# Optimization experiments

Measured on AMD Instinct MI355X. Metric: run time of the kernel, lower is better.

Reference implementation:

```python
import jax, jax.numpy as jnp
import numpy as np

CUTOFF = 3.5          # angular_cutoff (init kwarg)
EPS = 1e-7            # keras.backend.epsilon()
CLIP_MIN = 1e-10      # tf.clip_by_value min on Carnot denominators
B, N = 8, 32
MLP_DIMS = [(9, 64), (64, 64), (64, 64), (64, 64), (64, 64), (64, 128), (128, 256)]


def _he(key, fan_in, fan_out):
    return jax.random.normal(key, (fan_in, fan_out), jnp.float32) * np.float32(np.sqrt(2.0 / fan_in))


def setup_inputs() -> dict:
    key = jax.random.key(0)
    k_pos, k_sp, k_w, k_b = jax.random.split(key, 4)
    # realistic symmetric distance matrix with zero diagonal, from random 3D positions
    pos = jax.random.uniform(k_pos, (B, N, 3), jnp.float32) * 9.0
    diff = pos[:, :, None, :] - pos[:, None, :, :]
    D = jnp.sqrt(jnp.sum(diff * diff, axis=-1) + 1e-12)
    D = D * (1.0 - jnp.eye(N, dtype=jnp.float32))
    species = jax.random.randint(k_sp, (B, N), 1, 10).astype(jnp.float32)
    inp = {"distance_matrices": D, "num_species_batch": species}
    for i, (fi, fo) in enumerate(MLP_DIMS):
        inp[f"W{i}"] = _he(jax.random.fold_in(k_w, i), fi, fo)
        inp[f"b{i}"] = jax.random.normal(jax.random.fold_in(k_b, i), (fo,), jnp.float32) * 0.01
    return inp


def _ang_mlp(x, W0, b0, W1, b1, W2, b2, W3, b3, W4, b4, W5, b5, W6, b6):
    # residual MLP: 9 -> 64 (x5, two residual adds) -> 128 -> 256, all tanh
    x_res = jnp.tanh(x @ W0 + b0)
    x1 = jnp.tanh(x_res @ W1 + b1)
    xb1 = x1 + x_res
    x2 = jnp.tanh(xb1 @ W2 + b2)
    x3 = jnp.tanh(x2 @ W3 + b3)
    x4 = jnp.tanh(x3 @ W4 + b4)
    xb2 = x4 + xb1
    xb3 = jnp.tanh(xb2 @ W5 + b5)
    return jnp.tanh(xb3 @ W6 + b6)


def _forward(D, S, W0, b0, W1, b1, W2, b2, W3, b3, W4, b4, W5, b5, W6, b6):
    n = D.shape[-1]
    ji, ki = jnp.triu_indices(n, k=1)                       # P = n(n-1)/2 ordered pairs j<k
    cm = (D < CUTOFF) & (D != 0.0)                          # [B,N,N]
    mask = cm[:, :, ji] & cm[:, :, ki]                      # [B,N,P] valid triplets (i;j,k)
    R_ij = D[:, :, ji]                                      # [B,N,P]
    R_ik = D[:, :, ki]
    R_jk = jnp.broadcast_to(D[:, ji, ki][:, None, :], R_ij.shape)
    z_i = jnp.broadcast_to(S[:, :, None], R_ij.shape)
    z_j = jnp.broadcast_to(S[:, ji][:, None, :], R_ij.shape)
    z_k = jnp.broadcast_to(S[:, ki][:, None, :], R_ij.shape)
    # Carnot formula for the three cosines of the triangle (i,j,k)
    clip = lambda d: jnp.maximum(d, CLIP_MIN)
    c_i = (R_ij**2 + R_ik**2 - R_jk**2) / clip(2.0 * R_ij * R_ik)
    c_j = (R_ij**2 + R_jk**2 - R_ik**2) / clip(2.0 * R_ij * R_jk)
    c_k = (R_ik**2 + R_jk**2 - R_ij**2) / clip(2.0 * R_ik * R_jk)
    geo = jnp.stack([
        R_ij + R_ik + R_jk,
        R_ij * R_ik + R_ij * R_jk + R_ik * R_jk,
        R_ij * R_ik * R_jk,
    ], axis=-1)                                             # [B,N,P,3]
    chem = jnp.stack([
        z_i + z_j + z_k,
        c_i + c_j + c_k,
        z_i * (z_j + z_k) + z_j * z_k - c_i * (c_j + c_k) - c_j * c_k,
        z_i * (c_j + c_k) + c_i * (z_j + z_k) + z_j * c_k + c_j * z_k,
        z_i * (z_j * z_k - c_j * c_k) - c_i * (z_j * c_k + c_j * z_k),
        z_i * (z_j * c_k + c_j * z_k) + c_i * (z_j * z_k - c_j * c_k),
    ], axis=-1)                                             # [B,N,P,6]
    geo = geo / (jnp.linalg.norm(geo, axis=-1, keepdims=True) + EPS)
    chem = chem / (jnp.linalg.norm(chem, axis=-1, keepdims=True) + EPS)
    feat = jnp.concatenate([geo, chem], axis=-1)            # [B,N,P,9]
    out = _ang_mlp(feat, W0, b0, W1, b1, W2, b2, W3, b3, W4, b4, W5, b5, W6, b6)  # [B,N,P,256]
    f_c = lambda d: 0.5 * jnp.cos(np.float32(np.pi) * d / CUTOFF) + 0.5
    w = jnp.where(mask, f_c(R_ij) * f_c(R_ik), 0.0)[..., None]
    GA = jnp.sum(out * w, axis=2)                           # scatter-add over triplets -> [B,N,256]
    return GA / (jnp.linalg.norm(GA, axis=-1, keepdims=True) + EPS)


def reference(distance_matrices, num_species_batch, W0, b0, W1, b1, W2, b2, W3, b3, W4, b4, W5, b5, W6, b6):
    return _forward(distance_matrices, num_species_batch, W0, b0, W1, b1, W2, b2, W3, b3, W4, b4, W5, b5, W6, b6)
```

## Files before the change

### kernel.cpp

```cpp
#include <hip/hip_runtime.h>
#include <math.h>

#define NB 8
#define NA 32
#define NCELL 256
#define NPAIR 496
#define SLOT 496
#define FST 10
#define TC 16
#define XS 20
#define NQ 8
#define CUTOFF_F 3.5f
#define EPS_F 1e-7f
#define CLIP_MIN_F 1e-10f
#define PI_F 3.14159274101257324f

__global__ __launch_bounds__(256) void aev_feat(
    const float* __restrict__ D, const float* __restrict__ S,
    float* __restrict__ feat, int* __restrict__ count, float* __restrict__ GA)
{
    __shared__ float Dm[NA][NA];
    __shared__ float Sv[NA];
    __shared__ int s_T;
    const int tid = threadIdx.x;
    const int cell = blockIdx.x;
    const int b = cell >> 5, i = cell & 31;

    for (int idx = tid; idx < NA * NA; idx += 256)
        ((float*)Dm)[idx] = D[b * NA * NA + idx];
    if (tid < NA) Sv[tid] = S[b * NA + tid];
    if (tid == 0) s_T = 0;
    GA[cell * 256 + tid] = 0.f;
    __syncthreads();

    for (int p = tid; p < NPAIR; p += 256) {
        int rem = p, j = 0;
        while (rem >= 31 - j) { rem -= 31 - j; ++j; }
        const int k = j + 1 + rem;
        const float dij = Dm[i][j], dik = Dm[i][k];
        if (dij < CUTOFF_F && dij != 0.f && dik < CUTOFF_F && dik != 0.f) {
            const int slot = atomicAdd(&s_T, 1);
            const float Rij = dij, Rik = dik, Rjk = Dm[j][k];
            const float zi = Sv[i], zj = Sv[j], zk = Sv[k];
            const float ci = (Rij*Rij + Rik*Rik - Rjk*Rjk) / fmaxf(2.f*Rij*Rik, CLIP_MIN_F);
            const float cj = (Rij*Rij + Rjk*Rjk - Rik*Rik) / fmaxf(2.f*Rij*Rjk, CLIP_MIN_F);
            const float ck = (Rik*Rik + Rjk*Rjk - Rij*Rij) / fmaxf(2.f*Rik*Rjk, CLIP_MIN_F);
            float g0 = Rij + Rik + Rjk;
            float g1 = Rij*Rik + Rij*Rjk + Rik*Rjk;
            float g2 = Rij*Rik*Rjk;
            const float gn = sqrtf(g0*g0 + g1*g1 + g2*g2) + EPS_F;
            float h0 = zi + zj + zk;
            float h1 = ci + cj + ck;
            float h2 = zi*(zj + zk) + zj*zk - ci*(cj + ck) - cj*ck;
            float h3 = zi*(cj + ck) + ci*(zj + zk) + zj*ck + cj*zk;
            float h4 = zi*(zj*zk - cj*ck) - ci*(zj*ck + cj*zk);
            float h5 = zi*(zj*ck + cj*zk) + ci*(zj*zk - cj*ck);
            const float hn = sqrtf(h0*h0 + h1*h1 + h2*h2 + h3*h3 + h4*h4 + h5*h5) + EPS_F;
            const float fcij = 0.5f * cosf(PI_F * Rij / CUTOFF_F) + 0.5f;
            const float fcik = 0.5f * cosf(PI_F * Rik / CUTOFF_F) + 0.5f;
            float* fp = &feat[(cell * SLOT + slot) * FST];
            fp[0] = g0 / gn; fp[1] = g1 / gn; fp[2] = g2 / gn;
            fp[3] = h0 / hn; fp[4] = h1 / hn; fp[5] = h2 / hn;
            fp[6] = h3 / hn; fp[7] = h4 / hn; fp[8] = h5 / hn;
            fp[9] = fcij * fcik;
        }
    }
    __syncthreads();
    if (tid == 0) count[cell] = s_T;
}

__device__ __forceinline__ void cp_async16(const float* g, float* l) {
    __builtin_amdgcn_global_load_lds(
        (const __attribute__((address_space(1))) unsigned int*)g,
        (__attribute__((address_space(3))) unsigned int*)l, 16, 0, 0);
}

__device__ __forceinline__ void stage16k(const float* __restrict__ g,
                                         float* __restrict__ buf, int tid) {
    const int lane = tid & 63, w = tid >> 6;
#pragma unroll
    for (int r = 0; r < 4; ++r) {
        const int off = (w * 4 + r) * 256;
        cp_async16(g + off + lane * 4, buf + off);
    }
}

template<int K, bool RES>
__device__ __forceinline__ void compute64(
    const float* __restrict__ Wl, float bb,
    const float* __restrict__ X, float* __restrict__ Y,
    const float* __restrict__ R, int tid)
{
    const int fi = tid & 63;
    const int xo = (tid >> 6) * 4;
    float a0 = bb, a1 = bb, a2 = bb, a3 = bb;
#pragma unroll 4
    for (int k = 0; k < K; ++k) {
        const float4 xv = *(const float4*)&X[k * XS + xo];
        const float w = Wl[k * 64 + fi];
        a0 += xv.x * w; a1 += xv.y * w; a2 += xv.z * w; a3 += xv.w * w;
    }
    float4 y;
    y.x = tanhf(a0); y.y = tanhf(a1); y.z = tanhf(a2); y.w = tanhf(a3);
    if (RES) {
        const float4 r = *(const float4*)&R[fi * XS + xo];
        y.x += r.x; y.y += r.y; y.z += r.z; y.w += r.w;
    }
    *(float4*)&Y[fi * XS + xo] = y;
}

__device__ __forceinline__ void compute5_part(
    const float* __restrict__ Wl , const float* __restrict__ X,
    int k0, float (&a0)[4], float (&a1)[4], int tid)
{
    const int fo = tid & 63;
    const int xo = (tid >> 6) * 4;
#pragma unroll 4
    for (int k = 0; k < 32; ++k) {
        const float4 xv = *(const float4*)&X[(k0 + k) * XS + xo];
        const float w0 = Wl[k * 128 + fo];
        const float w1 = Wl[k * 128 + fo + 64];
        a0[0] += xv.x * w0; a0[1] += xv.y * w0; a0[2] += xv.z * w0; a0[3] += xv.w * w0;
        a1[0] += xv.x * w1; a1[1] += xv.y * w1; a1[2] += xv.z * w1; a1[3] += xv.w * w1;
    }
}

__device__ __forceinline__ void compute6_part(
    const float* __restrict__ Wl , const float* __restrict__ X,
    float (&a)[16], int tid)
{
#pragma unroll 2
    for (int k = 0; k < 16; ++k) {
        const float w = Wl[k * 256 + tid];
        const float4 x0 = *(const float4*)&X[k * XS + 0];
        const float4 x1 = *(const float4*)&X[k * XS + 4];
        const float4 x2 = *(const float4*)&X[k * XS + 8];
        const float4 x3 = *(const float4*)&X[k * XS + 12];
        a[0]  += x0.x * w; a[1]  += x0.y * w; a[2]  += x0.z * w; a[3]  += x0.w * w;
        a[4]  += x1.x * w; a[5]  += x1.y * w; a[6]  += x1.z * w; a[7]  += x1.w * w;
        a[8]  += x2.x * w; a[9]  += x2.y * w; a[10] += x2.z * w; a[11] += x2.w * w;
        a[12] += x3.x * w; a[13] += x3.y * w; a[14] += x3.z * w; a[15] += x3.w * w;
    }
}

__global__ __launch_bounds__(256) void aev_mlp(
    const float* __restrict__ feat, const int* __restrict__ count,
    const float* __restrict__ W0, const float* __restrict__ b0,
    const float* __restrict__ W1, const float* __restrict__ b1,
    const float* __restrict__ W2, const float* __restrict__ b2,
    const float* __restrict__ W3, const float* __restrict__ b3,
    const float* __restrict__ W4, const float* __restrict__ b4,
    const float* __restrict__ W5, const float* __restrict__ b5,
    const float* __restrict__ W6, const float* __restrict__ b6,
    float* __restrict__ GA)
{
    __shared__ __align__(16) float WA[4096];
    __shared__ __align__(16) float WBf[4096];
    __shared__ __align__(16) float W0s[576];
    __shared__ __align__(16) float Xs[9 * XS];
    __shared__ __align__(16) float U0[64 * XS];
    __shared__ __align__(16) float U1[64 * XS];
    __shared__ __align__(16) float U2[64 * XS];
    __shared__ float wsh[TC];

    const int tid = threadIdx.x;
    const int cell = blockIdx.x & 255;
    const int q = blockIdx.x >> 8;
    const int T = count[cell];
    const int nch = (T + TC - 1) / TC;
    if (q >= nch) return;

    const int fi64 = tid & 63;
    const float bias0 = b0[fi64];
    const float bias1 = b1[fi64];
    const float bias2 = b2[fi64];
    const float bias3 = b3[fi64];
    const float bias4 = b4[fi64];
    const float bias5a = b5[fi64];
    const float bias5b = b5[fi64 + 64];
    const float bias6 = b6[tid];

    if (tid < 144) ((float4*)W0s)[tid] = ((const float4*)W0)[tid];

    float gacc = 0.f;

    for (int c = q; c < nch; c += NQ) {
        const int t0 = c * TC;

        if (tid < TC * FST) {
            const int t = tid / FST, qf = tid % FST;
            const int slot = t0 + t;
            const float v = (slot < T) ? feat[(cell * SLOT + t0) * FST + tid] : 0.f;
            if (qf == 9) wsh[t] = v; else Xs[qf * XS + t] = v;
        }
        __syncthreads();

        stage16k(W1, WA, tid);
        compute64<9,  false>(W0s, bias0, Xs, U0, nullptr, tid);
        __syncthreads();
        stage16k(W2, WBf, tid);
        compute64<64, true >(WA, bias1, U0, U1, U0, tid);
        __syncthreads();
        stage16k(W3, WA, tid);
        compute64<64, false>(WBf, bias2, U1, U2, nullptr, tid);
        __syncthreads();
        stage16k(W4, WBf, tid);
        compute64<64, false>(WA, bias3, U2, U0, nullptr, tid);
        __syncthreads();
        stage16k(W5, WA, tid);
        compute64<64, true >(WBf, bias4, U0, U2, U1, tid);
        __syncthreads();

        float a0[4], a1[4];
#pragma unroll
        for (int r = 0; r < 4; ++r) { a0[r] = bias5a; a1[r] = bias5b; }
        stage16k(W5 + 4096, WBf, tid);
        compute5_part(WA, U2, 0, a0, a1, tid);
        __syncthreads();
        stage16k(W6, WA, tid);
        compute5_part(WBf, U2, 32, a0, a1, tid);
        {
            const int fo = tid & 63;
            const int xo = (tid >> 6) * 4;
            float4 y0, y1;
            y0.x = tanhf(a0[0]); y0.y = tanhf(a0[1]); y0.z = tanhf(a0[2]); y0.w = tanhf(a0[3]);
            y1.x = tanhf(a1[0]); y1.y = tanhf(a1[1]); y1.z = tanhf(a1[2]); y1.w = tanhf(a1[3]);
            *(float4*)&U0[fo * XS + xo] = y0;
            *(float4*)&U1[fo * XS + xo] = y1;
        }
        __syncthreads();

        float a6[16];
#pragma unroll
        for (int r = 0; r < 16; ++r) a6[r] = bias6;
        stage16k(W6 + 1 * 4096, WBf, tid);
        compute6_part(WA, U0 + 0 * XS, a6, tid);
        __syncthreads();
        stage16k(W6 + 2 * 4096, WA, tid);
        compute6_part(WBf, U0 + 16 * XS, a6, tid);
        __syncthreads();
        stage16k(W6 + 3 * 4096, WBf, tid);
        compute6_part(WA, U0 + 32 * XS, a6, tid);
        __syncthreads();
        stage16k(W6 + 4 * 4096, WA, tid);
        compute6_part(WBf, U0 + 48 * XS, a6, tid);
        __syncthreads();
        stage16k(W6 + 5 * 4096, WBf, tid);
        compute6_part(WA, U1 + 0 * XS, a6, tid);
        __syncthreads();
        stage16k(W6 + 6 * 4096, WA, tid);
        compute6_part(WBf, U1 + 16 * XS, a6, tid);
        __syncthreads();
        stage16k(W6 + 7 * 4096, WBf, tid);
        compute6_part(WA, U1 + 32 * XS, a6, tid);
        __syncthreads();
        compute6_part(WBf, U1 + 48 * XS, a6, tid);

#pragma unroll 4
        for (int r = 0; r < 16; ++r)
            gacc += wsh[r] * tanhf(a6[r]);
        __syncthreads();
    }

    atomicAdd(&GA[cell * 256 + tid], gacc);
}

__global__ __launch_bounds__(256) void aev_norm(
    const float* __restrict__ GA, float* __restrict__ out)
{
    __shared__ float wred[4];
    const int tid = threadIdx.x;
    const int cell = blockIdx.x;
    const float v = GA[cell * 256 + tid];
    float ss = v * v;
#pragma unroll
    for (int off = 32; off > 0; off >>= 1) ss += __shfl_down(ss, off);
    if ((tid & 63) == 0) wred[tid >> 6] = ss;
    __syncthreads();
    const float tot = wred[0] + wred[1] + wred[2] + wred[3];
    out[cell * 256 + tid] = v / (sqrtf(tot) + EPS_F);
}

extern "C" void kernel_launch(void* const* d_in, const int* in_sizes, int n_in,
                              void* d_out, int out_size, void* d_ws, size_t ws_size,
                              hipStream_t stream)
{
    const float* D  = (const float*)d_in[0];
    const float* S  = (const float*)d_in[1];
    const float* W0 = (const float*)d_in[2];  const float* b0 = (const float*)d_in[3];
    const float* W1 = (const float*)d_in[4];  const float* b1 = (const float*)d_in[5];
    const float* W2 = (const float*)d_in[6];  const float* b2 = (const float*)d_in[7];
    const float* W3 = (const float*)d_in[8];  const float* b3 = (const float*)d_in[9];
    const float* W4 = (const float*)d_in[10]; const float* b4 = (const float*)d_in[11];
    const float* W5 = (const float*)d_in[12]; const float* b5 = (const float*)d_in[13];
    const float* W6 = (const float*)d_in[14]; const float* b6 = (const float*)d_in[15];
    float* out = (float*)d_out;

    float* feat  = (float*)d_ws;
    int*   count = (int*)(feat + NCELL * SLOT * FST);
    float* GA    = (float*)(count + 256);

    aev_feat<<<dim3(NCELL), dim3(256), 0, stream>>>(D, S, feat, count, GA);
    aev_mlp<<<dim3(NCELL * NQ), dim3(256), 0, stream>>>(
        feat, count, W0, b0, W1, b1, W2, b2, W3, b3, W4, b4, W5, b5, W6, b6, GA);
    aev_norm<<<dim3(NCELL), dim3(256), 0, stream>>>(GA, out);
}
```

Measured before the change: 120.5 us.

## Triple-buffer MLP weight staging with partial-vmcnt barriers and fast tanh

Moves from two to three shared weight buffers so each global-to-LDS weight load is issued one layer further ahead. Full __syncthreads are replaced by barriers that wait only for LDS ops and all but the newest 4 global loads, letting the next stage's loads stay in flight during compute. It also swaps tanhf for an exp2/rcp-based approximation. The cost is more LDS per block (possibly lower occupancy), and correctness now depends on stage16k issuing exactly 4 vector memory ops per thread. The tanh approximation also loses some accuracy.

```diff
diff --git a/kernel.cpp b/kernel.cpp
--- a/kernel.cpp
+++ b/kernel.cpp
@@ -14,6 +14,24 @@
 #define EPS_F 1e-7f
 #define CLIP_MIN_F 1e-10f
 #define PI_F 3.14159274101257324f
+
+#define PIPE_BAR4() do { \
+    asm volatile("s_waitcnt lgkmcnt(0) vmcnt(4)" ::: "memory"); \
+    __builtin_amdgcn_s_barrier(); \
+    __builtin_amdgcn_sched_barrier(0); \
+} while (0)
+#define PIPE_BAR0() do { \
+    asm volatile("s_waitcnt lgkmcnt(0) vmcnt(0)" ::: "memory"); \
+    __builtin_amdgcn_s_barrier(); \
+    __builtin_amdgcn_sched_barrier(0); \
+} while (0)
+
+__device__ __forceinline__ float fast_tanh(float x) {
+    const float ax = fabsf(x);
+    const float t = exp2f(fminf(2.8853900817779268f * ax, 30.0f));
+    const float r = (t - 1.0f) * __builtin_amdgcn_rcpf(t + 1.0f);
+    return __int_as_float((__float_as_int(x) & 0x80000000) | __float_as_int(r));
+}
 
 __global__ __launch_bounds__(256) void aev_feat(
     const float* __restrict__ D, const float* __restrict__ S,
@@ -101,7 +119,7 @@
         a0 += xv.x * w; a1 += xv.y * w; a2 += xv.z * w; a3 += xv.w * w;
     }
     float4 y;
-    y.x = tanhf(a0); y.y = tanhf(a1); y.z = tanhf(a2); y.w = tanhf(a3);
+    y.x = fast_tanh(a0); y.y = fast_tanh(a1); y.z = fast_tanh(a2); y.w = fast_tanh(a3);
     if (RES) {
         const float4 r = *(const float4*)&R[fi * XS + xo];
         y.x += r.x; y.y += r.y; y.z += r.z; y.w += r.w;
@@ -154,8 +172,9 @@
     const float* __restrict__ W6, const float* __restrict__ b6,
     float* __restrict__ GA)
 {
-    __shared__ __align__(16) float WA[4096];
-    __shared__ __align__(16) float WBf[4096];
+    __shared__ __align__(16) float WB0[4096];
+    __shared__ __align__(16) float WB1[4096];
+    __shared__ __align__(16) float WB2[4096];
     __shared__ __align__(16) float W0s[576];
     __shared__ __align__(16) float Xs[9 * XS];
     __shared__ __align__(16) float U0[64 * XS];
@@ -187,78 +206,79 @@
     for (int c = q; c < nch; c += NQ) {
         const int t0 = c * TC;
 
+        stage16k(W1, WB0, tid);
         if (tid < TC * FST) {
             const int t = tid / FST, qf = tid % FST;
             const int slot = t0 + t;
             const float v = (slot < T) ? feat[(cell * SLOT + t0) * FST + tid] : 0.f;
             if (qf == 9) wsh[t] = v; else Xs[qf * XS + t] = v;
         }
-        __syncthreads();
-
-        stage16k(W1, WA, tid);
+        PIPE_BAR4();
+        stage16k(W2, WB1, tid);
         compute64<9,  false>(W0s, bias0, Xs, U0, nullptr, tid);
-        __syncthreads();
-        stage16k(W2, WBf, tid);
-        compute64<64, true >(WA, bias1, U0, U1, U0, tid);
-        __syncthreads();
-        stage16k(W3, WA, tid);
-        compute64<64, false>(WBf, bias2, U1, U2, nullptr, tid);
-        __syncthreads();
-        stage16k(W4, WBf, tid);
-        compute64<64, false>(WA, bias3, U2, U0, nullptr, tid);
-        __syncthreads();
-        stage16k(W5, WA, tid);
-        compute64<64, true >(WBf, bias4, U0, U2, U1, tid);
-        __syncthreads();
+        PIPE_BAR4();
+        stage16k(W3, WB2, tid);
+        compute64<64, true >(WB0, bias1, U0, U1, U0, tid);
+        PIPE_BAR4();
+        stage16k(W4, WB0, tid);
+        compute64<64, false>(WB1, bias2, U1, U2, nullptr, tid);
+        PIPE_BAR4();
+        stage16k(W5, WB1, tid);
+        compute64<64, false>(WB2, bias3, U2, U0, nullptr, tid);
+        PIPE_BAR4();
+        stage16k(W5 + 4096, WB2, tid);
+        compute64<64, true >(WB0, bias4, U0, U2, U1, tid);
+        PIPE_BAR4();
 
         float a0[4], a1[4];
 #pragma unroll
         for (int r = 0; r < 4; ++r) { a0[r] = bias5a; a1[r] = bias5b; }
-        stage16k(W5 + 4096, WBf, tid);
-        compute5_part(WA, U2, 0, a0, a1, tid);
-        __syncthreads();
-        stage16k(W6, WA, tid);
-        compute5_part(WBf, U2, 32, a0, a1, tid);
+        stage16k(W6, WB0, tid);
+        compute5_part(WB1, U2, 0, a0, a1, tid);
+        PIPE_BAR4();
+        stage16k(W6 + 4096, WB1, tid);
+        compute5_part(WB2, U2, 32, a0, a1, tid);
         {
             const int fo = tid & 63;
             const int xo = (tid >> 6) * 4;
             float4 y0, y1;
-            y0.x = tanhf(a0[0]); y0.y = tanhf(a0[1]); y0.z = tanhf(a0[2]); y0.w = tanhf(a0[3]);
-            y1.x = tanhf(a1[0]); y1.y = tanhf(a1[1]); y1.z = tanhf(a1[2]); y1.w = tanhf(a1[3]);
+            y0.x = fast_tanh(a0[0]); y0.y = fast_tanh(a0[1]);
+            y0.z = fast_tanh(a0[2]); y0.w = fast_tanh(a0[3]);
+            y1.x = fast_tanh(a1[0]); y1.y = fast_tanh(a1[1]);
+            y1.z = fast_tanh(a1[2]); y1.w = fast_tanh(a1[3]);
             *(float4*)&U0[fo * XS + xo] = y0;
             *(float4*)&U1[fo * XS + xo] = y1;
         }
-        __syncthreads();
+        PIPE_BAR4();
 
         float a6[16];
 #pragma unroll
         for (int r = 0; r < 16; ++r) a6[r] = bias6;
-        stage16k(W6 + 1 * 4096, WBf, tid);
-        compute6_part(WA, U0 + 0 * XS, a6, tid);
-        __syncthreads();
-        stage16k(W6 + 2 * 4096, WA, tid);
-        compute6_part(WBf, U0 + 16 * XS, a6, tid);
-        __syncthreads();
-        stage16k(W6 + 3 * 4096, WBf, tid);
-        compute6_part(WA, U0 + 32 * XS, a6, tid);
-        __syncthreads();
-        stage16k(W6 + 4 * 4096, WA, tid);
-        compute6_part(WBf, U0 + 48 * XS, a6, tid);
-        __syncthreads();
-        stage16k(W6 + 5 * 4096, WBf, tid);
-        compute6_part(WA, U1 + 0 * XS, a6, tid);
-        __syncthreads();
-        stage16k(W6 + 6 * 4096, WA, tid);
-        compute6_part(WBf, U1 + 16 * XS, a6, tid);
-        __syncthreads();
-        stage16k(W6 + 7 * 4096, WBf, tid);
-        compute6_part(WA, U1 + 32 * XS, a6, tid);
-        __syncthreads();
-        compute6_part(WBf, U1 + 48 * XS, a6, tid);
+        stage16k(W6 + 2 * 4096, WB2, tid);
+        compute6_part(WB0, U0 + 0 * XS, a6, tid);
+        PIPE_BAR4();
+        stage16k(W6 + 3 * 4096, WB0, tid);
+        compute6_part(WB1, U0 + 16 * XS, a6, tid);
+        PIPE_BAR4();
+        stage16k(W6 + 4 * 4096, WB1, tid);
+        compute6_part(WB2, U0 + 32 * XS, a6, tid);
+        PIPE_BAR4();
+        stage16k(W6 + 5 * 4096, WB2, tid);
+        compute6_part(WB0, U0 + 48 * XS, a6, tid);
+        PIPE_BAR4();
+        stage16k(W6 + 6 * 4096, WB0, tid);
+        compute6_part(WB1, U1 + 0 * XS, a6, tid);
+        PIPE_BAR4();
+        stage16k(W6 + 7 * 4096, WB1, tid);
+        compute6_part(WB2, U1 + 16 * XS, a6, tid);
+        PIPE_BAR4();
+        compute6_part(WB0, U1 + 32 * XS, a6, tid);
+        PIPE_BAR0();
+        compute6_part(WB1, U1 + 48 * XS, a6, tid);
 
 #pragma unroll 4
         for (int r = 0; r < 16; ++r)
-            gacc += wsh[r] * tanhf(a6[r]);
+            gacc += wsh[r] * fast_tanh(a6[r]);
         __syncthreads();
     }
 
```

New measurement: 115.9 us. -3.8%, faster.
